# Kernel tuning notes

Measured on AMD Instinct MI355X. Metric: run time of the kernel, lower is better.

Reference implementation:

```python
import jax, jax.numpy as jnp
import numpy as np

N = 50000   # num_nodes
E = 400000  # num_edges
IN, HID, OUT, H = 128, 64, 128, 4
GAT_HID = HID * H  # 256
EPS = 1e-5
NEG_SLOPE = 0.2


def setup_inputs() -> dict:
    key = jax.random.key(0)
    ks = jax.random.split(key, 24)

    def w(k, shape, fan_in):
        return (jax.random.normal(k, shape) * (1.0 / np.sqrt(fan_in))).astype(jnp.float32)

    x = jax.random.normal(ks[0], (N, IN), dtype=jnp.float32)
    edge_index = jax.random.randint(ks[1], (2, E), 0, N, dtype=jnp.int32)

    return {
        "x": x,
        "edge_index": edge_index,
        # GCN branch: layer1 IN->HID, layer2 HID->OUT
        "W_gcn1": w(ks[2], (IN, HID), IN), "b_gcn1": jnp.zeros((HID,), jnp.float32),
        "W_gcn2": w(ks[3], (HID, OUT), HID), "b_gcn2": jnp.zeros((OUT,), jnp.float32),
        # GAT branch: layer1 IN -> H heads x HID (concat), layer2 GAT_HID -> H heads x OUT (mean)
        "W_gat1": w(ks[4], (IN, H * HID), IN),
        "a_src1": w(ks[5], (H, HID), HID), "a_dst1": w(ks[6], (H, HID), HID),
        "b_gat1": jnp.zeros((H * HID,), jnp.float32),
        "W_gat2": w(ks[7], (GAT_HID, H * OUT), GAT_HID),
        "a_src2": w(ks[8], (H, OUT), OUT), "a_dst2": w(ks[9], (H, OUT), OUT),
        "b_gat2": jnp.zeros((OUT,), jnp.float32),
        # LayerNorms
        "g_gcn": jnp.ones((OUT,), jnp.float32), "bt_gcn": jnp.zeros((OUT,), jnp.float32),
        "g_gat": jnp.ones((OUT,), jnp.float32), "bt_gat": jnp.zeros((OUT,), jnp.float32),
        # projected_concat fusion
        "W_fuse": w(ks[10], (2 * OUT, OUT), 2 * OUT), "b_fuse": jnp.zeros((OUT,), jnp.float32),
    }


def _with_self_loops(src, dst, n):
    loop = jnp.arange(n, dtype=src.dtype)
    return jnp.concatenate([src, loop]), jnp.concatenate([dst, loop])


def _gcn_layer(x, W, b, src, dst, n):
    # PyG GCNConv: x' = D^{-1/2}(A+I)D^{-1/2} X W + b
    xw = x @ W
    s, d = _with_self_loops(src, dst, n)
    deg = jax.ops.segment_sum(jnp.ones_like(s, dtype=xw.dtype), d, num_segments=n)
    dis = jnp.where(deg > 0, jax.lax.rsqrt(jnp.maximum(deg, 1.0)), 0.0)
    norm = dis[s] * dis[d]                      # [E2]
    msg = norm[:, None] * xw[s]                 # [E2, C]
    return jax.ops.segment_sum(msg, d, num_segments=n) + b


def _segment_softmax(e, seg, n):
    m = jax.ops.segment_max(e, seg, num_segments=n)
    ee = jnp.exp(e - m[seg])
    den = jax.ops.segment_sum(ee, seg, num_segments=n)
    return ee / den[seg]


def _gat_layer(x, W, a_src, a_dst, b, src, dst, n, heads, out_ch, concat):
    xh = (x @ W).reshape(n, heads, out_ch)      # [N, H, C]
    alpha_s = jnp.einsum('nhc,hc->nh', xh, a_src)
    alpha_d = jnp.einsum('nhc,hc->nh', xh, a_dst)
    s, d = _with_self_loops(src, dst, n)
    e = jax.nn.leaky_relu(alpha_s[s] + alpha_d[d], NEG_SLOPE)   # [E2, H]
    alpha = _segment_softmax(e, d, n)                           # [E2, H]
    out = jax.ops.segment_sum(alpha[:, :, None] * xh[s], d, num_segments=n)  # [N,H,C]
    if concat:
        return out.reshape(n, heads * out_ch) + b
    return out.mean(axis=1) + b


def _layer_norm(x, g, b):
    mu = x.mean(axis=-1, keepdims=True)
    var = ((x - mu) ** 2).mean(axis=-1, keepdims=True)
    return (x - mu) * jax.lax.rsqrt(var + EPS) * g + b


def reference(x, edge_index,
              W_gcn1, b_gcn1, W_gcn2, b_gcn2,
              W_gat1, a_src1, a_dst1, b_gat1,
              W_gat2, a_src2, a_dst2, b_gat2,
              g_gcn, bt_gcn, g_gat, bt_gat,
              W_fuse, b_fuse):
    src, dst = edge_index[0], edge_index[1]
    n = x.shape[0]
    # GCN branch (relu between layers, dropout p=0.0 -> identity)
    h = jax.nn.relu(_gcn_layer(x, W_gcn1, b_gcn1, src, dst, n))
    x_gcn = _gcn_layer(h, W_gcn2, b_gcn2, src, dst, n)
    # GAT branch (elu between layers)
    g1 = _gat_layer(x, W_gat1, a_src1, a_dst1, b_gat1, src, dst, n, H, HID, True)
    g1 = jax.nn.elu(g1)
    x_gat = _gat_layer(g1, W_gat2, a_src2, a_dst2, b_gat2, src, dst, n, H, OUT, False)
    # Norm + projected_concat fusion
    x_gcn = _layer_norm(x_gcn, g_gcn, bt_gcn)
    x_gat = _layer_norm(x_gat, g_gat, bt_gat)
    x_cat = jnp.concatenate([x_gcn, x_gat], axis=-1)
    return x_cat @ W_fuse + b_fuse
```

## Files before the change

kernel.cpp:

```cpp
#include <hip/hip_runtime.h>
#include <cmath>

static constexpr float EPS = 1e-5f;
static constexpr float NEG = 0.2f;

typedef __attribute__((ext_vector_type(8))) short short8v;
typedef __attribute__((ext_vector_type(4))) short short4v;
typedef __attribute__((ext_vector_type(4))) float f32x4;

__device__ inline unsigned short f2bf(float f) {
    union { float f; unsigned u; } v; v.f = f;
    unsigned r = v.u + 0x7FFF + ((v.u >> 16) & 1);
    return (unsigned short)(r >> 16);
}
__device__ inline float bf2f(unsigned short u) {
    union { unsigned u; float f; } v; v.u = (unsigned)u << 16; return v.f;
}

__global__ void count_kernel(const int* __restrict__ ei, int* __restrict__ cnt, int E) {
    int e = blockIdx.x * 256 + threadIdx.x;
    if (e < E) atomicAdd(&cnt[ei[E + e]], 1);
}

__global__ __launch_bounds__(256) void partial_kernel(const int* __restrict__ cnt,
                                                      int* __restrict__ partials, int n) {
    int tid = threadIdx.x, lane = tid & 63, wid = tid >> 6;
    int base = blockIdx.x * 1024 + tid * 4;
    int s = 0;
    if (base + 3 < n) {
        int4 v = *reinterpret_cast<const int4*>(&cnt[base]);
        s = v.x + v.y + v.z + v.w;
    } else {
        for (int j = 0; j < 4; j++) if (base + j < n) s += cnt[base + j];
    }
    #pragma unroll
    for (int o = 32; o; o >>= 1) s += __shfl_xor(s, o, 64);
    __shared__ int ws[4];
    if (lane == 0) ws[wid] = s;
    __syncthreads();
    if (tid == 0) partials[blockIdx.x] = ws[0] + ws[1] + ws[2] + ws[3];
}

__global__ void scanp_kernel(int* __restrict__ partials, int nb) {
    int lane = threadIdx.x;
    int v = (lane < nb) ? partials[lane] : 0;
    int s = v;
    #pragma unroll
    for (int o = 1; o < 64; o <<= 1) {
        int t = __shfl_up(s, o, 64);
        if (lane >= o) s += t;
    }
    if (lane < nb) partials[lane] = s - v;
}

__global__ __launch_bounds__(256) void scan2_kernel(const int* __restrict__ cnt,
                                                    const int* __restrict__ partials,
                                                    int* __restrict__ rowptr,
                                                    int* __restrict__ cursor,
                                                    float* __restrict__ dis, int n, int E) {
    int tid = threadIdx.x, lane = tid & 63, wid = tid >> 6;
    int base = blockIdx.x * 1024 + tid * 4;
    int v[4]; int s = 0;
    #pragma unroll
    for (int j = 0; j < 4; j++) { v[j] = (base + j < n) ? cnt[base + j] : 0; s += v[j]; }
    int ts = s;
    #pragma unroll
    for (int o = 1; o < 64; o <<= 1) {
        int t = __shfl_up(ts, o, 64);
        if (lane >= o) ts += t;
    }
    __shared__ int wsum[4];
    if (lane == 63) wsum[wid] = ts;
    __syncthreads();
    int woff = 0;
    for (int w = 0; w < wid; w++) woff += wsum[w];
    int excl = ts - s + woff + partials[blockIdx.x];
    #pragma unroll
    for (int j = 0; j < 4; j++) {
        int idx = base + j;
        if (idx < n) {
            rowptr[idx] = excl;
            cursor[idx] = excl;
            dis[idx] = rsqrtf((float)(v[j] + 1));
            excl += v[j];
        }
    }
    if (blockIdx.x == 0 && tid == 0) rowptr[n] = E;
}

__global__ void fill_kernel(const int* __restrict__ ei, int* __restrict__ cursor,
                            int* __restrict__ col, int E) {
    int e = blockIdx.x * 256 + threadIdx.x;
    if (e < E) {
        int d = ei[E + e];
        int pos = atomicAdd(&cursor[d], 1);
        col[pos] = ei[e];
    }
}

__global__ void convert_x_kernel(const float* __restrict__ x, unsigned short* __restrict__ xb, int total4) {
    int i = blockIdx.x * 256 + threadIdx.x;
    if (i < total4) {
        float4 v = *reinterpret_cast<const float4*>(&x[(size_t)i * 4]);
        unsigned long long pk = (unsigned long long)f2bf(v.x)
                              | ((unsigned long long)f2bf(v.y) << 16)
                              | ((unsigned long long)f2bf(v.z) << 32)
                              | ((unsigned long long)f2bf(v.w) << 48);
        *reinterpret_cast<unsigned long long*>(&xb[(size_t)i * 4]) = pk;
    }
}

__global__ void convert_weights_kernel(const float* W1, const float* W2, const float* W3,
                                       const float* W4, const float* W5,
                                       unsigned short* T1, unsigned short* T2, unsigned short* T3,
                                       unsigned short* T4, unsigned short* T5) {
    int idx = blockIdx.x * 256 + threadIdx.x;
    const float* S; unsigned short* D; int K, C, off;
    if      (idx <   8192) { S = W1; D = T1; K = 128; C =  64; off = 0; }
    else if (idx <  16384) { S = W2; D = T2; K =  64; C = 128; off = 8192; }
    else if (idx <  49152) { S = W3; D = T3; K = 128; C = 256; off = 16384; }
    else if (idx < 180224) { S = W4; D = T4; K = 256; C = 512; off = 49152; }
    else if (idx < 212992) { S = W5; D = T5; K = 256; C = 128; off = 180224; }
    else return;
    int j = idx - off;
    int c = j / K, k = j % K;
    D[j] = f2bf(S[(size_t)k * C + c]);
}

template<int K, int C, bool OBF>
__global__ __launch_bounds__(256) void mfma_gemm(const unsigned short* __restrict__ A,
                                                 const unsigned short* __restrict__ WT,
                                                 const float* __restrict__ bias,
                                                 void* __restrict__ outp, int M) {
    constexpr int BM = 128, BN = 64, BK = 64;
    __shared__ unsigned short As[BM * BK];
    __shared__ unsigned short Ws[BN * BK];
    int tid = threadIdx.x;
    int wid = tid >> 6, lane = tid & 63;
    int m0 = blockIdx.x * BM;
    int n0 = blockIdx.y * BN;

    f32x4 acc[2][4] = {};

    for (int k0 = 0; k0 < K; k0 += BK) {
        for (int i = tid; i < BM * (BK / 8); i += 256) {
            int row = i >> 3;
            int kk = (i & 7) * 8;
            int gr = m0 + row;
            short8v v = short8v{0, 0, 0, 0, 0, 0, 0, 0};
            if (gr < M) v = *reinterpret_cast<const short8v*>(&A[(size_t)gr * K + k0 + kk]);
            int byte = (kk * 2) ^ ((row & 7) << 4);
            *reinterpret_cast<short8v*>((char*)As + row * (BK * 2) + byte) = v;
        }
        for (int i = tid; i < BN * (BK / 8); i += 256) {
            int nrow = i >> 3;
            int kk = (i & 7) * 8;
            short8v v = *reinterpret_cast<const short8v*>(&WT[(size_t)(n0 + nrow) * K + k0 + kk]);
            int byte = (kk * 2) ^ ((nrow & 7) << 4);
            *reinterpret_cast<short8v*>((char*)Ws + nrow * (BK * 2) + byte) = v;
        }
        __syncthreads();
        #pragma unroll
        for (int kc = 0; kc < BK; kc += 32) {
            short8v afr[2], bfr[4];
            int kk = kc + (lane >> 4) * 8;
            #pragma unroll
            for (int mf = 0; mf < 2; mf++) {
                int row = wid * 32 + mf * 16 + (lane & 15);
                int byte = (kk * 2) ^ ((row & 7) << 4);
                afr[mf] = *reinterpret_cast<const short8v*>((char*)As + row * (BK * 2) + byte);
            }
            #pragma unroll
            for (int nf = 0; nf < 4; nf++) {
                int nrow = nf * 16 + (lane & 15);
                int byte = (kk * 2) ^ ((nrow & 7) << 4);
                bfr[nf] = *reinterpret_cast<const short8v*>((char*)Ws + nrow * (BK * 2) + byte);
            }
            #pragma unroll
            for (int mf = 0; mf < 2; mf++)
                #pragma unroll
                for (int nf = 0; nf < 4; nf++)
                    acc[mf][nf] = __builtin_amdgcn_mfma_f32_16x16x32_bf16(
                        afr[mf], bfr[nf], acc[mf][nf], 0, 0, 0);
        }
        __syncthreads();
    }
    #pragma unroll
    for (int mf = 0; mf < 2; mf++) {
        #pragma unroll
        for (int nf = 0; nf < 4; nf++) {
            #pragma unroll
            for (int r = 0; r < 4; r++) {
                int row = m0 + wid * 32 + mf * 16 + (lane >> 4) * 4 + r;
                int colg = n0 + nf * 16 + (lane & 15);
                if (row < M) {
                    float v = acc[mf][nf][r];
                    if (bias) v += bias[colg];
                    if constexpr (OBF)
                        ((unsigned short*)outp)[(size_t)row * C + colg] = f2bf(v);
                    else
                        ((float*)outp)[(size_t)row * C + colg] = v;
                }
            }
        }
    }
}

__global__ __launch_bounds__(256) void gcn_prop1_kernel(const unsigned short* __restrict__ xw,
                                                        const float* __restrict__ dis,
                                                        const int* __restrict__ rowptr,
                                                        const int* __restrict__ col,
                                                        const float* __restrict__ bias,
                                                        unsigned short* __restrict__ outp, int n) {
    int wid = threadIdx.x >> 6, lane = threadIdx.x & 63;
    int node = blockIdx.x * 4 + wid;
    if (node >= n) return;
    float dd = dis[node];
    float acc = dd * bf2f(xw[(size_t)node * 64 + lane]);
    int b0 = rowptr[node], b1 = rowptr[node + 1];
    for (int i = b0; i < b1; i++) {
        int s = col[i];
        acc += dis[s] * bf2f(xw[(size_t)s * 64 + lane]);
    }
    float r = dd * acc + bias[lane];
    r = fmaxf(r, 0.f);
    outp[(size_t)node * 64 + lane] = f2bf(r);
}

__global__ __launch_bounds__(256) void gcn_prop2_ln_kernel(const unsigned short* __restrict__ xw,
                                                           const float* __restrict__ dis,
                                                           const int* __restrict__ rowptr,
                                                           const int* __restrict__ col,
                                                           const float* __restrict__ bias,
                                                           const float* __restrict__ gw,
                                                           const float* __restrict__ gb,
                                                           unsigned short* __restrict__ catb, int n) {
    int wid = threadIdx.x >> 6, lane = threadIdx.x & 63;
    int node = blockIdx.x * 4 + wid;
    if (node >= n) return;
    float dd = dis[node];
    unsigned vs = *reinterpret_cast<const unsigned*>(&xw[(size_t)node * 128 + lane * 2]);
    float a0 = dd * bf2f((unsigned short)(vs & 0xFFFF));
    float a1 = dd * bf2f((unsigned short)(vs >> 16));
    int b0 = rowptr[node], b1 = rowptr[node + 1];
    for (int i = b0; i < b1; i++) {
        int s = col[i];
        float ds = dis[s];
        unsigned v = *reinterpret_cast<const unsigned*>(&xw[(size_t)s * 128 + lane * 2]);
        a0 += ds * bf2f((unsigned short)(v & 0xFFFF));
        a1 += ds * bf2f((unsigned short)(v >> 16));
    }
    float r0 = dd * a0 + bias[lane * 2];
    float r1 = dd * a1 + bias[lane * 2 + 1];
    float sm = r0 + r1, sq = r0 * r0 + r1 * r1;
    #pragma unroll
    for (int o = 1; o < 64; o <<= 1) { sm += __shfl_xor(sm, o, 64); sq += __shfl_xor(sq, o, 64); }
    float mu = sm * (1.f / 128.f);
    float var = sq * (1.f / 128.f) - mu * mu;
    float rs = rsqrtf(var + EPS);
    float o0 = (r0 - mu) * rs * gw[lane * 2] + gb[lane * 2];
    float o1 = (r1 - mu) * rs * gw[lane * 2 + 1] + gb[lane * 2 + 1];
    unsigned pk = (unsigned)f2bf(o0) | ((unsigned)f2bf(o1) << 16);
    *reinterpret_cast<unsigned*>(&catb[(size_t)node * 256 + lane * 2]) = pk;
}

template<int HC>
__global__ __launch_bounds__(256) void alpha_kernel(const unsigned short* __restrict__ xh,
                                                    const float* __restrict__ a_src,
                                                    const float* __restrict__ a_dst,
                                                    float* __restrict__ as_, float* __restrict__ ad_, int n) {
    constexpr int PL = HC / 16;
    int wid = threadIdx.x >> 6, lane = threadIdx.x & 63;
    int node = blockIdx.x * 4 + wid;
    if (node >= n) return;
    int head = lane >> 4, cb = (lane & 15) * PL;
    const unsigned short* xr = xh + (size_t)node * (4 * HC) + lane * PL;
    float ps = 0.f, pd = 0.f;
    #pragma unroll
    for (int j = 0; j < PL; j++) {
        float v = bf2f(xr[j]);
        ps += v * a_src[head * HC + cb + j];
        pd += v * a_dst[head * HC + cb + j];
    }
    #pragma unroll
    for (int o = 1; o < 16; o <<= 1) { ps += __shfl_xor(ps, o, 64); pd += __shfl_xor(pd, o, 64); }
    if ((lane & 15) == 0) {
        as_[(size_t)node * 4 + head] = ps;
        ad_[(size_t)node * 4 + head] = pd;
    }
}

__global__ __launch_bounds__(256) void gat_prop1_kernel(const unsigned short* __restrict__ xh,
                                                        const float* __restrict__ as_,
                                                        const float* __restrict__ ad_,
                                                        const int* __restrict__ rowptr,
                                                        const int* __restrict__ col,
                                                        const float* __restrict__ bias,
                                                        unsigned short* __restrict__ outp, int n) {
    constexpr int CAP = 96;
    __shared__ float ex[4][CAP][4];
    __shared__ int scol[4][CAP];
    int wid = threadIdx.x >> 6, lane = threadIdx.x & 63;
    int node = blockIdx.x * 4 + wid;
    if (node >= n) return;
    int b0 = rowptr[node];
    int cnt = rowptr[node + 1] - b0;
    float4 adv = *reinterpret_cast<const float4*>(&ad_[(size_t)node * 4]);
    float p0 = 0, p1 = 0, p2 = 0, p3 = 0;
    for (int i = lane; i <= cnt; i += 64) {
        int s = (i == cnt) ? node : col[b0 + i];
        float4 asv = *reinterpret_cast<const float4*>(&as_[(size_t)s * 4]);
        float e0 = asv.x + adv.x; e0 = e0 > 0.f ? e0 : NEG * e0; float x0 = __expf(e0);
        float e1 = asv.y + adv.y; e1 = e1 > 0.f ? e1 : NEG * e1; float x1 = __expf(e1);
        float e2 = asv.z + adv.z; e2 = e2 > 0.f ? e2 : NEG * e2; float x2 = __expf(e2);
        float e3 = asv.w + adv.w; e3 = e3 > 0.f ? e3 : NEG * e3; float x3 = __expf(e3);
        if (i < CAP) {
            ex[wid][i][0] = x0; ex[wid][i][1] = x1; ex[wid][i][2] = x2; ex[wid][i][3] = x3;
            scol[wid][i] = s;
        }
        p0 += x0; p1 += x1; p2 += x2; p3 += x3;
    }
    #pragma unroll
    for (int o = 1; o < 64; o <<= 1) {
        p0 += __shfl_xor(p0, o, 64); p1 += __shfl_xor(p1, o, 64);
        p2 += __shfl_xor(p2, o, 64); p3 += __shfl_xor(p3, o, 64);
    }
    __builtin_amdgcn_wave_barrier();
    int head = lane >> 4;
    float wsel = head == 0 ? 1.f / p0 : head == 1 ? 1.f / p1 : head == 2 ? 1.f / p2 : 1.f / p3;
    int coff = lane * 4;
    float fa0 = 0, fa1 = 0, fa2 = 0, fa3 = 0;
    for (int i = 0; i <= cnt; i++) {
        int s; float we;
        if (i < CAP) {
            s = scol[wid][i];
            we = ex[wid][i][head] * wsel;
        } else {
            s = (i == cnt) ? node : col[b0 + i];
            float4 asv = *reinterpret_cast<const float4*>(&as_[(size_t)s * 4]);
            float eh = head == 0 ? asv.x + adv.x : head == 1 ? asv.y + adv.y
                     : head == 2 ? asv.z + adv.z : asv.w + adv.w;
            eh = eh > 0.f ? eh : NEG * eh;
            we = __expf(eh) * wsel;
        }
        short4v v = *reinterpret_cast<const short4v*>(&xh[(size_t)s * 256 + coff]);
        fa0 += we * bf2f((unsigned short)v[0]);
        fa1 += we * bf2f((unsigned short)v[1]);
        fa2 += we * bf2f((unsigned short)v[2]);
        fa3 += we * bf2f((unsigned short)v[3]);
    }
    float r0 = fa0 + bias[coff];     r0 = r0 > 0.f ? r0 : __expf(r0) - 1.f;
    float r1 = fa1 + bias[coff + 1]; r1 = r1 > 0.f ? r1 : __expf(r1) - 1.f;
    float r2 = fa2 + bias[coff + 2]; r2 = r2 > 0.f ? r2 : __expf(r2) - 1.f;
    float r3 = fa3 + bias[coff + 3]; r3 = r3 > 0.f ? r3 : __expf(r3) - 1.f;
    short4v o4;
    o4[0] = (short)f2bf(r0); o4[1] = (short)f2bf(r1);
    o4[2] = (short)f2bf(r2); o4[3] = (short)f2bf(r3);
    *reinterpret_cast<short4v*>(&outp[(size_t)node * 256 + coff]) = o4;
}

__global__ __launch_bounds__(256) void gat_prop2_ln_kernel(const unsigned short* __restrict__ xh,
                                                           const float* __restrict__ as_,
                                                           const float* __restrict__ ad_,
                                                           const int* __restrict__ rowptr,
                                                           const int* __restrict__ col,
                                                           const float* __restrict__ bias,
                                                           const float* __restrict__ gw,
                                                           const float* __restrict__ gb,
                                                           unsigned short* __restrict__ catb, int n) {
    constexpr int CAP = 96;
    __shared__ float ex[4][CAP][4];
    __shared__ int scol[4][CAP];
    int wid = threadIdx.x >> 6, lane = threadIdx.x & 63;
    int node = blockIdx.x * 4 + wid;
    if (node >= n) return;
    int b0 = rowptr[node];
    int cnt = rowptr[node + 1] - b0;
    float4 adv = *reinterpret_cast<const float4*>(&ad_[(size_t)node * 4]);
    float p0 = 0, p1 = 0, p2 = 0, p3 = 0;
    for (int i = lane; i <= cnt; i += 64) {
        int s = (i == cnt) ? node : col[b0 + i];
        float4 asv = *reinterpret_cast<const float4*>(&as_[(size_t)s * 4]);
        float e0 = asv.x + adv.x; e0 = e0 > 0.f ? e0 : NEG * e0; float x0 = __expf(e0);
        float e1 = asv.y + adv.y; e1 = e1 > 0.f ? e1 : NEG * e1; float x1 = __expf(e1);
        float e2 = asv.z + adv.z; e2 = e2 > 0.f ? e2 : NEG * e2; float x2 = __expf(e2);
        float e3 = asv.w + adv.w; e3 = e3 > 0.f ? e3 : NEG * e3; float x3 = __expf(e3);
        if (i < CAP) {
            ex[wid][i][0] = x0; ex[wid][i][1] = x1; ex[wid][i][2] = x2; ex[wid][i][3] = x3;
            scol[wid][i] = s;
        }
        p0 += x0; p1 += x1; p2 += x2; p3 += x3;
    }
    #pragma unroll
    for (int o = 1; o < 64; o <<= 1) {
        p0 += __shfl_xor(p0, o, 64); p1 += __shfl_xor(p1, o, 64);
        p2 += __shfl_xor(p2, o, 64); p3 += __shfl_xor(p3, o, 64);
    }
    __builtin_amdgcn_wave_barrier();
    int head = lane >> 4;
    float wsel = head == 0 ? 0.25f / p0 : head == 1 ? 0.25f / p1 : head == 2 ? 0.25f / p2 : 0.25f / p3;
    int cw = (lane & 15) * 8;
    float facc[8] = {0, 0, 0, 0, 0, 0, 0, 0};
    for (int i = 0; i <= cnt; i++) {
        int s; float we;
        if (i < CAP) {
            s = scol[wid][i];
            we = ex[wid][i][head] * wsel;
        } else {
            s = (i == cnt) ? node : col[b0 + i];
            float4 asv = *reinterpret_cast<const float4*>(&as_[(size_t)s * 4]);
            float eh = head == 0 ? asv.x + adv.x : head == 1 ? asv.y + adv.y
                     : head == 2 ? asv.z + adv.z : asv.w + adv.w;
            eh = eh > 0.f ? eh : NEG * eh;
            we = __expf(eh) * wsel;
        }
        short8v v = *reinterpret_cast<const short8v*>(&xh[(size_t)s * 512 + lane * 8]);
        #pragma unroll
        for (int j = 0; j < 8; j++) facc[j] += we * bf2f((unsigned short)v[j]);
    }
    #pragma unroll
    for (int j = 0; j < 8; j++) {
        facc[j] += __shfl_xor(facc[j], 16, 64);
        facc[j] += __shfl_xor(facc[j], 32, 64);
        facc[j] += bias[cw + j];
    }
    float sm = 0, sq = 0;
    #pragma unroll
    for (int j = 0; j < 8; j++) { sm += facc[j]; sq += facc[j] * facc[j]; }
    #pragma unroll
    for (int o = 1; o < 16; o <<= 1) { sm += __shfl_xor(sm, o, 64); sq += __shfl_xor(sq, o, 64); }
    float mu = sm * (1.f / 128.f);
    float var = sq * (1.f / 128.f) - mu * mu;
    float rs = rsqrtf(var + EPS);
    if (lane < 16) {
        short8v o8;
        #pragma unroll
        for (int j = 0; j < 8; j++)
            o8[j] = (short)f2bf((facc[j] - mu) * rs * gw[cw + j] + gb[cw + j]);
        *reinterpret_cast<short8v*>(&catb[(size_t)node * 256 + 128 + cw]) = o8;
    }
}

extern "C" void kernel_launch(void* const* d_in, const int* in_sizes, int n_in,
                              void* d_out, int out_size, void* d_ws, size_t ws_size,
                              hipStream_t stream) {
    const float* x      = (const float*)d_in[0];
    const int*   ei     = (const int*)d_in[1];
    const float* W_gcn1 = (const float*)d_in[2];
    const float* b_gcn1 = (const float*)d_in[3];
    const float* W_gcn2 = (const float*)d_in[4];
    const float* b_gcn2 = (const float*)d_in[5];
    const float* W_gat1 = (const float*)d_in[6];
    const float* a_src1 = (const float*)d_in[7];
    const float* a_dst1 = (const float*)d_in[8];
    const float* b_gat1 = (const float*)d_in[9];
    const float* W_gat2 = (const float*)d_in[10];
    const float* a_src2 = (const float*)d_in[11];
    const float* a_dst2 = (const float*)d_in[12];
    const float* b_gat2 = (const float*)d_in[13];
    const float* g_gcn  = (const float*)d_in[14];
    const float* bt_gcn = (const float*)d_in[15];
    const float* g_gat  = (const float*)d_in[16];
    const float* bt_gat = (const float*)d_in[17];
    const float* W_fuse = (const float*)d_in[18];
    const float* b_fuse = (const float*)d_in[19];
    float* out = (float*)d_out;

    const int n = in_sizes[0] / 128;
    const int E = in_sizes[1] / 2;

    char* ws = (char*)d_ws;
    size_t off = 0;
    auto alloc = [&](size_t bytes) -> char* {
        char* p = ws + off;
        off += (bytes + 255) & ~(size_t)255;
        return p;
    };
    int*   cnt      = (int*)alloc((size_t)n * 4);
    int*   rowptr   = (int*)alloc((size_t)(n + 1) * 4);
    int*   cursor   = (int*)alloc((size_t)n * 4);
    int*   col      = (int*)alloc((size_t)E * 4);
    int*   partials = (int*)alloc(64 * 4);
    float* dis      = (float*)alloc((size_t)n * 4);
    float* as_      = (float*)alloc((size_t)n * 16);
    float* ad_      = (float*)alloc((size_t)n * 16);
    unsigned short* xb   = (unsigned short*)alloc((size_t)n * 128 * 2);
    unsigned short* WT1  = (unsigned short*)alloc(8192 * 2);
    unsigned short* WT2  = (unsigned short*)alloc(8192 * 2);
    unsigned short* WT3  = (unsigned short*)alloc(32768 * 2);
    unsigned short* WT4  = (unsigned short*)alloc(131072 * 2);
    unsigned short* WT5  = (unsigned short*)alloc(32768 * 2);
    unsigned short* xw1b = (unsigned short*)alloc((size_t)n * 64 * 2);
    unsigned short* hb   = (unsigned short*)alloc((size_t)n * 64 * 2);
    unsigned short* xw2b = (unsigned short*)alloc((size_t)n * 128 * 2);
    unsigned short* xh1b = (unsigned short*)alloc((size_t)n * 256 * 2);
    unsigned short* g1b  = (unsigned short*)alloc((size_t)n * 256 * 2);
    unsigned short* xh2b = (unsigned short*)alloc((size_t)n * 512 * 2);
    unsigned short* catb = (unsigned short*)alloc((size_t)n * 256 * 2);

    const int nb = (n + 1023) / 1024;

    hipMemsetAsync(cnt, 0, (size_t)n * 4, stream);
    count_kernel<<<(E + 255) / 256, 256, 0, stream>>>(ei, cnt, E);
    partial_kernel<<<nb, 256, 0, stream>>>(cnt, partials, n);
    scanp_kernel<<<1, 64, 0, stream>>>(partials, nb);
    scan2_kernel<<<nb, 256, 0, stream>>>(cnt, partials, rowptr, cursor, dis, n, E);
    fill_kernel<<<(E + 255) / 256, 256, 0, stream>>>(ei, cursor, col, E);
    convert_x_kernel<<<(n * 32 + 255) / 256, 256, 0, stream>>>(x, xb, n * 32);
    convert_weights_kernel<<<(212992 + 255) / 256, 256, 0, stream>>>(
        W_gcn1, W_gcn2, W_gat1, W_gat2, W_fuse, WT1, WT2, WT3, WT4, WT5);

    int gm = (n + 127) / 128;
    int gn4 = (n + 3) / 4;

    mfma_gemm<128, 64, true><<<dim3(gm, 1), 256, 0, stream>>>(xb, WT1, nullptr, xw1b, n);
    gcn_prop1_kernel<<<gn4, 256, 0, stream>>>(xw1b, dis, rowptr, col, b_gcn1, hb, n);
    mfma_gemm<64, 128, true><<<dim3(gm, 2), 256, 0, stream>>>(hb, WT2, nullptr, xw2b, n);
    gcn_prop2_ln_kernel<<<gn4, 256, 0, stream>>>(xw2b, dis, rowptr, col, b_gcn2, g_gcn, bt_gcn, catb, n);

    mfma_gemm<128, 256, true><<<dim3(gm, 4), 256, 0, stream>>>(xb, WT3, nullptr, xh1b, n);
    alpha_kernel<64><<<gn4, 256, 0, stream>>>(xh1b, a_src1, a_dst1, as_, ad_, n);
    gat_prop1_kernel<<<gn4, 256, 0, stream>>>(xh1b, as_, ad_, rowptr, col, b_gat1, g1b, n);
    mfma_gemm<256, 512, true><<<dim3(gm, 8), 256, 0, stream>>>(g1b, WT4, nullptr, xh2b, n);
    alpha_kernel<128><<<gn4, 256, 0, stream>>>(xh2b, a_src2, a_dst2, as_, ad_, n);
    gat_prop2_ln_kernel<<<gn4, 256, 0, stream>>>(xh2b, as_, ad_, rowptr, col, b_gat2, g_gat, bt_gat, catb, n);

    mfma_gemm<256, 128, false><<<dim3(gm, 2), 256, 0, stream>>>(catb, WT5, b_fuse, out, n);
}
```

Baseline: 394.3 us.

## Reorder GAT layers to aggregate first, then transform with fused epilogues

Both GAT layers now aggregate neighbour features before the linear projection, instead of projecting and then aggregating. The gather per edge therefore runs over the narrower input width (128 and 256) rather than the projected width (256 and 512). Attention logits are computed straight from the inputs using precomputed products of W and the attention vectors. ELU, bias, head mean and LayerNorm are folded into the following GEMM epilogues. In exchange, per-head aggregated buffers as wide as 1024 bf16 per node must be written and read, and the second GEMM's K grows to 1024.

Result: slower. 444.8 us (+12.8%).

```diff
diff --git a/kernel.cpp b/kernel.cpp
--- a/kernel.cpp
+++ b/kernel.cpp
@@ -113,18 +113,47 @@
 __global__ void convert_weights_kernel(const float* W1, const float* W2, const float* W3,
                                        const float* W4, const float* W5,
                                        unsigned short* T1, unsigned short* T2, unsigned short* T3,
-                                       unsigned short* T4, unsigned short* T5) {
+                                       unsigned short* TF, unsigned short* T5) {
     int idx = blockIdx.x * 256 + threadIdx.x;
-    const float* S; unsigned short* D; int K, C, off;
-    if      (idx <   8192) { S = W1; D = T1; K = 128; C =  64; off = 0; }
-    else if (idx <  16384) { S = W2; D = T2; K =  64; C = 128; off = 8192; }
-    else if (idx <  49152) { S = W3; D = T3; K = 128; C = 256; off = 16384; }
-    else if (idx < 180224) { S = W4; D = T4; K = 256; C = 512; off = 49152; }
-    else if (idx < 212992) { S = W5; D = T5; K = 256; C = 128; off = 180224; }
-    else return;
-    int j = idx - off;
-    int c = j / K, k = j % K;
-    D[j] = f2bf(S[(size_t)k * C + c]);
+    if (idx < 8192) {
+        int j = idx, c = j / 128, k = j % 128;
+        T1[j] = f2bf(W1[(size_t)k * 64 + c]);
+    } else if (idx < 16384) {
+        int j = idx - 8192, c = j / 64, k = j % 64;
+        T2[j] = f2bf(W2[(size_t)k * 128 + c]);
+    } else if (idx < 49152) {
+        int j = idx - 16384, c = j / 128, k = j % 128;
+        T3[j] = f2bf(W3[(size_t)k * 256 + c]);
+    } else if (idx < 180224) {
+        int j = idx - 49152;
+        int c = j / 1024, kk = j % 1024, h = kk >> 8, k = kk & 255;
+        TF[j] = f2bf(0.25f * W4[(size_t)k * 512 + h * 128 + c]);
+    } else if (idx < 212992) {
+        int j = idx - 180224, c = j / 256, k = j % 256;
+        T5[j] = f2bf(W5[(size_t)k * 128 + c]);
+    }
+}
+
+__global__ void walpha_kernel(const float* __restrict__ W1, const float* __restrict__ as1,
+                              const float* __restrict__ ad1,
+                              const float* __restrict__ W2, const float* __restrict__ as2,
+                              const float* __restrict__ ad2,
+                              float* __restrict__ wa1, float* __restrict__ wa2) {
+    int idx = blockIdx.x * 256 + threadIdx.x;
+    if (idx < 1024) {
+        int k = idx >> 3, t = idx & 7, h = t >> 1;
+        const float* a = (t & 1) ? ad1 : as1;
+        float s = 0.f;
+        for (int c = 0; c < 64; c++) s += W1[(size_t)k * 256 + h * 64 + c] * a[h * 64 + c];
+        wa1[idx] = s;
+    } else if (idx < 3072) {
+        int j = idx - 1024;
+        int k = j >> 3, t = j & 7, h = t >> 1;
+        const float* a = (t & 1) ? ad2 : as2;
+        float s = 0.f;
+        for (int c = 0; c < 128; c++) s += W2[(size_t)k * 512 + h * 128 + c] * a[h * 128 + c];
+        wa2[j] = s;
+    }
 }
 
 template<int K, int C, bool OBF>
@@ -201,6 +230,174 @@
                     else
                         ((float*)outp)[(size_t)row * C + colg] = v;
                 }
+            }
+        }
+    }
+}
+
+__global__ __launch_bounds__(256) void gemm_head_kernel(const unsigned short* __restrict__ A,
+                                                        const unsigned short* __restrict__ WT3,
+                                                        const float* __restrict__ bias,
+                                                        unsigned short* __restrict__ g1b, int M) {
+    constexpr int BM = 128, BK = 64, K = 128;
+    int head = blockIdx.y;
+    __shared__ unsigned short As[BM * BK];
+    __shared__ unsigned short Ws[64 * BK];
+    int tid = threadIdx.x;
+    int wid = tid >> 6, lane = tid & 63;
+    int m0 = blockIdx.x * BM;
+
+    f32x4 acc[2][4] = {};
+
+    for (int k0 = 0; k0 < K; k0 += BK) {
+        for (int i = tid; i < BM * (BK / 8); i += 256) {
+            int row = i >> 3;
+            int kk = (i & 7) * 8;
+            int gr = m0 + row;
+            short8v v = short8v{0, 0, 0, 0, 0, 0, 0, 0};
+            if (gr < M) v = *reinterpret_cast<const short8v*>(&A[(size_t)gr * 512 + head * 128 + k0 + kk]);
+            int byte = (kk * 2) ^ ((row & 7) << 4);
+            *reinterpret_cast<short8v*>((char*)As + row * (BK * 2) + byte) = v;
+        }
+        for (int i = tid; i < 64 * (BK / 8); i += 256) {
+            int nrow = i >> 3;
+            int kk = (i & 7) * 8;
+            short8v v = *reinterpret_cast<const short8v*>(&WT3[(size_t)(head * 64 + nrow) * 128 + k0 + kk]);
+            int byte = (kk * 2) ^ ((nrow & 7) << 4);
+            *reinterpret_cast<short8v*>((char*)Ws + nrow * (BK * 2) + byte) = v;
+        }
+        __syncthreads();
+        #pragma unroll
+        for (int kc = 0; kc < BK; kc += 32) {
+            short8v afr[2], bfr[4];
+            int kk = kc + (lane >> 4) * 8;
+            #pragma unroll
+            for (int mf = 0; mf < 2; mf++) {
+                int row = wid * 32 + mf * 16 + (lane & 15);
+                int byte = (kk * 2) ^ ((row & 7) << 4);
+                afr[mf] = *reinterpret_cast<const short8v*>((char*)As + row * (BK * 2) + byte);
+            }
+            #pragma unroll
+            for (int nf = 0; nf < 4; nf++) {
+                int nrow = nf * 16 + (lane & 15);
+                int byte = (kk * 2) ^ ((nrow & 7) << 4);
+                bfr[nf] = *reinterpret_cast<const short8v*>((char*)Ws + nrow * (BK * 2) + byte);
+            }
+            #pragma unroll
+            for (int mf = 0; mf < 2; mf++)
+                #pragma unroll
+                for (int nf = 0; nf < 4; nf++)
+                    acc[mf][nf] = __builtin_amdgcn_mfma_f32_16x16x32_bf16(
+                        afr[mf], bfr[nf], acc[mf][nf], 0, 0, 0);
+        }
+        __syncthreads();
+    }
+    #pragma unroll
+    for (int mf = 0; mf < 2; mf++) {
+        #pragma unroll
+        for (int nf = 0; nf < 4; nf++) {
+            #pragma unroll
+            for (int r = 0; r < 4; r++) {
+                int row = m0 + wid * 32 + mf * 16 + (lane >> 4) * 4 + r;
+                int cl = head * 64 + nf * 16 + (lane & 15);
+                if (row < M) {
+                    float v = acc[mf][nf][r] + bias[cl];
+                    v = v > 0.f ? v : __expf(v) - 1.f;
+                    g1b[(size_t)row * 256 + cl] = f2bf(v);
+                }
+            }
+        }
+    }
+}
+
+template<int K>
+__global__ __launch_bounds__(256) void gemm_ln_kernel(const unsigned short* __restrict__ A,
+                                                      const unsigned short* __restrict__ WT,
+                                                      const float* __restrict__ bias,
+                                                      const float* __restrict__ gw,
+                                                      const float* __restrict__ gb,
+                                                      unsigned short* __restrict__ catb,
+                                                      int coloff, int M) {
+    constexpr int BM = 128, BN = 128, BK = 64;
+    __shared__ unsigned short As[BM * BK];
+    __shared__ unsigned short Ws[BN * BK];
+    int tid = threadIdx.x;
+    int wid = tid >> 6, lane = tid & 63;
+    int m0 = blockIdx.x * BM;
+
+    f32x4 acc[2][8] = {};
+
+    for (int k0 = 0; k0 < K; k0 += BK) {
+        for (int i = tid; i < BM * (BK / 8); i += 256) {
+            int row = i >> 3;
+            int kk = (i & 7) * 8;
+            int gr = m0 + row;
+            short8v v = short8v{0, 0, 0, 0, 0, 0, 0, 0};
+            if (gr < M) v = *reinterpret_cast<const short8v*>(&A[(size_t)gr * K + k0 + kk]);
+            int byte = (kk * 2) ^ ((row & 7) << 4);
+            *reinterpret_cast<short8v*>((char*)As + row * (BK * 2) + byte) = v;
+        }
+        for (int i = tid; i < BN * (BK / 8); i += 256) {
+            int nrow = i >> 3;
+            int kk = (i & 7) * 8;
+            short8v v = *reinterpret_cast<const short8v*>(&WT[(size_t)nrow * K + k0 + kk]);
+            int byte = (kk * 2) ^ ((nrow & 7) << 4);
+            *reinterpret_cast<short8v*>((char*)Ws + nrow * (BK * 2) + byte) = v;
+        }
+        __syncthreads();
+        #pragma unroll
+        for (int kc = 0; kc < BK; kc += 32) {
+            short8v afr[2], bfr[8];
+            int kk = kc + (lane >> 4) * 8;
+            #pragma unroll
+            for (int mf = 0; mf < 2; mf++) {
+                int row = wid * 32 + mf * 16 + (lane & 15);
+                int byte = (kk * 2) ^ ((row & 7) << 4);
+                afr[mf] = *reinterpret_cast<const short8v*>((char*)As + row * (BK * 2) + byte);
+            }
+            #pragma unroll
+            for (int nf = 0; nf < 8; nf++) {
+                int nrow = nf * 16 + (lane & 15);
+                int byte = (kk * 2) ^ ((nrow & 7) << 4);
+                bfr[nf] = *reinterpret_cast<const short8v*>((char*)Ws + nrow * (BK * 2) + byte);
+            }
+            #pragma unroll
+            for (int mf = 0; mf < 2; mf++)
+                #pragma unroll
+                for (int nf = 0; nf < 8; nf++)
+                    acc[mf][nf] = __builtin_amdgcn_mfma_f32_16x16x32_bf16(
+                        afr[mf], bfr[nf], acc[mf][nf], 0, 0, 0);
+        }
+        __syncthreads();
+    }
+    int cb = lane & 15;
+    float gwv[8], gbv[8], bv[8];
+    #pragma unroll
+    for (int nf = 0; nf < 8; nf++) {
+        int c = nf * 16 + cb;
+        gwv[nf] = gw[c]; gbv[nf] = gb[c]; bv[nf] = bias[c];
+    }
+    #pragma unroll
+    for (int mf = 0; mf < 2; mf++) {
+        #pragma unroll
+        for (int r = 0; r < 4; r++) {
+            int row = m0 + wid * 32 + mf * 16 + (lane >> 4) * 4 + r;
+            float v[8]; float sm = 0.f, sq = 0.f;
+            #pragma unroll
+            for (int nf = 0; nf < 8; nf++) {
+                v[nf] = acc[mf][nf][r] + bv[nf];
+                sm += v[nf]; sq += v[nf] * v[nf];
+            }
+            #pragma unroll
+            for (int o = 1; o < 16; o <<= 1) { sm += __shfl_xor(sm, o, 64); sq += __shfl_xor(sq, o, 64); }
+            float mu = sm * (1.f / 128.f);
+            float var = sq * (1.f / 128.f) - mu * mu;
+            float rs = rsqrtf(var + EPS);
+            if (row < M) {
+                #pragma unroll
+                for (int nf = 0; nf < 8; nf++)
+                    catb[(size_t)row * 256 + coloff + nf * 16 + cb] =
+                        f2bf((v[nf] - mu) * rs * gwv[nf] + gbv[nf]);
             }
         }
     }
@@ -264,39 +461,44 @@
     *reinterpret_cast<unsigned*>(&catb[(size_t)node * 256 + lane * 2]) = pk;
 }
 
-template<int HC>
-__global__ __launch_bounds__(256) void alpha_kernel(const unsigned short* __restrict__ xh,
-                                                    const float* __restrict__ a_src,
-                                                    const float* __restrict__ a_dst,
-                                                    float* __restrict__ as_, float* __restrict__ ad_, int n) {
-    constexpr int PL = HC / 16;
+template<int K>
+__global__ __launch_bounds__(256) void alpha_x_kernel(const unsigned short* __restrict__ F,
+                                                      const float* __restrict__ wa,
+                                                      float* __restrict__ as_, float* __restrict__ ad_, int n) {
+    constexpr int PL = K / 64;
     int wid = threadIdx.x >> 6, lane = threadIdx.x & 63;
     int node = blockIdx.x * 4 + wid;
     if (node >= n) return;
-    int head = lane >> 4, cb = (lane & 15) * PL;
-    const unsigned short* xr = xh + (size_t)node * (4 * HC) + lane * PL;
-    float ps = 0.f, pd = 0.f;
+    float p[8] = {0, 0, 0, 0, 0, 0, 0, 0};
+    const unsigned short* fr = F + (size_t)node * K + lane * PL;
     #pragma unroll
     for (int j = 0; j < PL; j++) {
-        float v = bf2f(xr[j]);
-        ps += v * a_src[head * HC + cb + j];
-        pd += v * a_dst[head * HC + cb + j];
-    }
-    #pragma unroll
-    for (int o = 1; o < 16; o <<= 1) { ps += __shfl_xor(ps, o, 64); pd += __shfl_xor(pd, o, 64); }
-    if ((lane & 15) == 0) {
-        as_[(size_t)node * 4 + head] = ps;
-        ad_[(size_t)node * 4 + head] = pd;
-    }
-}
-
-__global__ __launch_bounds__(256) void gat_prop1_kernel(const unsigned short* __restrict__ xh,
-                                                        const float* __restrict__ as_,
-                                                        const float* __restrict__ ad_,
-                                                        const int* __restrict__ rowptr,
-                                                        const int* __restrict__ col,
-                                                        const float* __restrict__ bias,
-                                                        unsigned short* __restrict__ outp, int n) {
+        float v = bf2f(fr[j]);
+        const float4* w4 = reinterpret_cast<const float4*>(wa + (size_t)(lane * PL + j) * 8);
+        float4 wA = w4[0], wB = w4[1];
+        p[0] += v * wA.x; p[1] += v * wA.y; p[2] += v * wA.z; p[3] += v * wA.w;
+        p[4] += v * wB.x; p[5] += v * wB.y; p[6] += v * wB.z; p[7] += v * wB.w;
+    }
+    #pragma unroll
+    for (int o = 1; o < 64; o <<= 1) {
+        #pragma unroll
+        for (int t = 0; t < 8; t++) p[t] += __shfl_xor(p[t], o, 64);
+    }
+    if (lane == 0) {
+        #pragma unroll
+        for (int t = 0; t < 8; t++) {
+            if (t & 1) ad_[(size_t)node * 4 + (t >> 1)] = p[t];
+            else       as_[(size_t)node * 4 + (t >> 1)] = p[t];
+        }
+    }
+}
+
+__global__ __launch_bounds__(256) void gat_agg1_kernel(const unsigned short* __restrict__ xb,
+                                                       const float* __restrict__ as_,
+                                                       const float* __restrict__ ad_,
+                                                       const int* __restrict__ rowptr,
+                                                       const int* __restrict__ col,
+                                                       unsigned short* __restrict__ agg, int n) {
     constexpr int CAP = 96;
     __shared__ float ex[4][CAP][4];
     __shared__ int scol[4][CAP];
@@ -326,48 +528,45 @@
         p2 += __shfl_xor(p2, o, 64); p3 += __shfl_xor(p3, o, 64);
     }
     __builtin_amdgcn_wave_barrier();
-    int head = lane >> 4;
-    float wsel = head == 0 ? 1.f / p0 : head == 1 ? 1.f / p1 : head == 2 ? 1.f / p2 : 1.f / p3;
-    int coff = lane * 4;
-    float fa0 = 0, fa1 = 0, fa2 = 0, fa3 = 0;
+    float inv0 = 1.f / p0, inv1 = 1.f / p1, inv2 = 1.f / p2, inv3 = 1.f / p3;
+    float ac[4][2] = {};
     for (int i = 0; i <= cnt; i++) {
-        int s; float we;
+        int s; float w0, w1, w2, w3;
         if (i < CAP) {
             s = scol[wid][i];
-            we = ex[wid][i][head] * wsel;
+            float4 e = *reinterpret_cast<const float4*>(&ex[wid][i][0]);
+            w0 = e.x * inv0; w1 = e.y * inv1; w2 = e.z * inv2; w3 = e.w * inv3;
         } else {
             s = (i == cnt) ? node : col[b0 + i];
             float4 asv = *reinterpret_cast<const float4*>(&as_[(size_t)s * 4]);
-            float eh = head == 0 ? asv.x + adv.x : head == 1 ? asv.y + adv.y
-                     : head == 2 ? asv.z + adv.z : asv.w + adv.w;
-            eh = eh > 0.f ? eh : NEG * eh;
-            we = __expf(eh) * wsel;
-        }
-        short4v v = *reinterpret_cast<const short4v*>(&xh[(size_t)s * 256 + coff]);
-        fa0 += we * bf2f((unsigned short)v[0]);
-        fa1 += we * bf2f((unsigned short)v[1]);
-        fa2 += we * bf2f((unsigned short)v[2]);
-        fa3 += we * bf2f((unsigned short)v[3]);
-    }
-    float r0 = fa0 + bias[coff];     r0 = r0 > 0.f ? r0 : __expf(r0) - 1.f;
-    float r1 = fa1 + bias[coff + 1]; r1 = r1 > 0.f ? r1 : __expf(r1) - 1.f;
-    float r2 = fa2 + bias[coff + 2]; r2 = r2 > 0.f ? r2 : __expf(r2) - 1.f;
-    float r3 = fa3 + bias[coff + 3]; r3 = r3 > 0.f ? r3 : __expf(r3) - 1.f;
-    short4v o4;
-    o4[0] = (short)f2bf(r0); o4[1] = (short)f2bf(r1);
-    o4[2] = (short)f2bf(r2); o4[3] = (short)f2bf(r3);
-    *reinterpret_cast<short4v*>(&outp[(size_t)node * 256 + coff]) = o4;
-}
-
-__global__ __launch_bounds__(256) void gat_prop2_ln_kernel(const unsigned short* __restrict__ xh,
-                                                           const float* __restrict__ as_,
-                                                           const float* __restrict__ ad_,
-                                                           const int* __restrict__ rowptr,
-                                                           const int* __restrict__ col,
-                                                           const float* __restrict__ bias,
-                                                           const float* __restrict__ gw,
-                                                           const float* __restrict__ gb,
-                                                           unsigned short* __restrict__ catb, int n) {
+            float e0 = asv.x + adv.x; e0 = e0 > 0.f ? e0 : NEG * e0;
+            float e1 = asv.y + adv.y; e1 = e1 > 0.f ? e1 : NEG * e1;
+            float e2 = asv.z + adv.z; e2 = e2 > 0.f ? e2 : NEG * e2;
+            float e3 = asv.w + adv.w; e3 = e3 > 0.f ? e3 : NEG * e3;
+            w0 = __expf(e0) * inv0; w1 = __expf(e1) * inv1;
+            w2 = __expf(e2) * inv2; w3 = __expf(e3) * inv3;
+        }
+        unsigned v = *reinterpret_cast<const unsigned*>(&xb[(size_t)s * 128 + lane * 2]);
+        float f0 = bf2f((unsigned short)(v & 0xFFFF));
+        float f1 = bf2f((unsigned short)(v >> 16));
+        ac[0][0] += w0 * f0; ac[0][1] += w0 * f1;
+        ac[1][0] += w1 * f0; ac[1][1] += w1 * f1;
+        ac[2][0] += w2 * f0; ac[2][1] += w2 * f1;
+        ac[3][0] += w3 * f0; ac[3][1] += w3 * f1;
+    }
+    #pragma unroll
+    for (int h = 0; h < 4; h++) {
+        unsigned pk = (unsigned)f2bf(ac[h][0]) | ((unsigned)f2bf(ac[h][1]) << 16);
+        *reinterpret_cast<unsigned*>(&agg[(size_t)node * 512 + h * 128 + lane * 2]) = pk;
+    }
+}
+
+__global__ __launch_bounds__(256) void gat_agg2_kernel(const unsigned short* __restrict__ g1b,
+                                                       const float* __restrict__ as_,
+                                                       const float* __restrict__ ad_,
+                                                       const int* __restrict__ rowptr,
+                                                       const int* __restrict__ col,
+                                                       unsigned short* __restrict__ agg, int n) {
     constexpr int CAP = 96;
     __shared__ float ex[4][CAP][4];
     __shared__ int scol[4][CAP];
@@ -397,47 +596,40 @@
         p2 += __shfl_xor(p2, o, 64); p3 += __shfl_xor(p3, o, 64);
     }
     __builtin_amdgcn_wave_barrier();
-    int head = lane >> 4;
-    float wsel = head == 0 ? 0.25f / p0 : head == 1 ? 0.25f / p1 : head == 2 ? 0.25f / p2 : 0.25f / p3;
-    int cw = (lane & 15) * 8;
-    float facc[8] = {0, 0, 0, 0, 0, 0, 0, 0};
+    float inv0 = 1.f / p0, inv1 = 1.f / p1, inv2 = 1.f / p2, inv3 = 1.f / p3;
+    float ac[4][4] = {};
     for (int i = 0; i <= cnt; i++) {
-        int s; float we;
+        int s; float w0, w1, w2, w3;
         if (i < CAP) {
             s = scol[wid][i];
-            we = ex[wid][i][head] * wsel;
+            float4 e = *reinterpret_cast<const float4*>(&ex[wid][i][0]);
+            w0 = e.x * inv0; w1 = e.y * inv1; w2 = e.z * inv2; w3 = e.w * inv3;
         } else {
             s = (i == cnt) ? node : col[b0 + i];
             float4 asv = *reinterpret_cast<const float4*>(&as_[(size_t)s * 4]);
-            float eh = head == 0 ? asv.x + adv.x : head == 1 ? asv.y + adv.y
-                     : head == 2 ? asv.z + adv.z : asv.w + adv.w;
-            eh = eh > 0.f ? eh : NEG * eh;
-            we = __expf(eh) * wsel;
-        }
-        short8v v = *reinterpret_cast<const short8v*>(&xh[(size_t)s * 512 + lane * 8]);
-        #pragma unroll
-        for (int j = 0; j < 8; j++) facc[j] += we * bf2f((unsigned short)v[j]);
-    }
-    #pragma unroll
-    for (int j = 0; j < 8; j++) {
-        facc[j] += __shfl_xor(facc[j], 16, 64);
-        facc[j] += __shfl_xor(facc[j], 32, 64);
-        facc[j] += bias[cw + j];
-    }
-    float sm = 0, sq = 0;
-    #pragma unroll
-    for (int j = 0; j < 8; j++) { sm += facc[j]; sq += facc[j] * facc[j]; }
-    #pragma unroll
-    for (int o = 1; o < 16; o <<= 1) { sm += __shfl_xor(sm, o, 64); sq += __shfl_xor(sq, o, 64); }
-    float mu = sm * (1.f / 128.f);
-    float var = sq * (1.f / 128.f) - mu * mu;
-    float rs = rsqrtf(var + EPS);
-    if (lane < 16) {
-        short8v o8;
-        #pragma unroll
-        for (int j = 0; j < 8; j++)
-            o8[j] = (short)f2bf((facc[j] - mu) * rs * gw[cw + j] + gb[cw + j]);
-        *reinterpret_cast<short8v*>(&catb[(size_t)node * 256 + 128 + cw]) = o8;
+            float e0 = asv.x + adv.x; e0 = e0 > 0.f ? e0 : NEG * e0;
+            float e1 = asv.y + adv.y; e1 = e1 > 0.f ? e1 : NEG * e1;
+            float e2 = asv.z + adv.z; e2 = e2 > 0.f ? e2 : NEG * e2;
+            float e3 = asv.w + adv.w; e3 = e3 > 0.f ? e3 : NEG * e3;
+            w0 = __expf(e0) * inv0; w1 = __expf(e1) * inv1;
+            w2 = __expf(e2) * inv2; w3 = __expf(e3) * inv3;
+        }
+        short4v v = *reinterpret_cast<const short4v*>(&g1b[(size_t)s * 256 + lane * 4]);
+        float f0 = bf2f((unsigned short)v[0]);
+        float f1 = bf2f((unsigned short)v[1]);
+        float f2 = bf2f((unsigned short)v[2]);
+        float f3 = bf2f((unsigned short)v[3]);
+        ac[0][0] += w0 * f0; ac[0][1] += w0 * f1; ac[0][2] += w0 * f2; ac[0][3] += w0 * f3;
+        ac[1][0] += w1 * f0; ac[1][1] += w1 * f1; ac[1][2] += w1 * f2; ac[1][3] += w1 * f3;
+        ac[2][0] += w2 * f0; ac[2][1] += w2 * f1; ac[2][2] += w2 * f2; ac[2][3] += w2 * f3;
+        ac[3][0] += w3 * f0; ac[3][1] += w3 * f1; ac[3][2] += w3 * f2; ac[3][3] += w3 * f3;
+    }
+    #pragma unroll
+    for (int h = 0; h < 4; h++) {
+        short4v o4;
+        o4[0] = (short)f2bf(ac[h][0]); o4[1] = (short)f2bf(ac[h][1]);
+        o4[2] = (short)f2bf(ac[h][2]); o4[3] = (short)f2bf(ac[h][3]);
+        *reinterpret_cast<short4v*>(&agg[(size_t)node * 1024 + h * 256 + lane * 4]) = o4;
     }
 }
 
@@ -484,18 +676,21 @@
     float* dis      = (float*)alloc((size_t)n * 4);
     float* as_      = (float*)alloc((size_t)n * 16);
     float* ad_      = (float*)alloc((size_t)n * 16);
+    float* wa1      = (float*)alloc(1024 * 4);
+    float* wa2      = (float*)alloc(2048 * 4);
     unsigned short* xb   = (unsigned short*)alloc((size_t)n * 128 * 2);
     unsigned short* WT1  = (unsigned short*)alloc(8192 * 2);
     unsigned short* WT2  = (unsigned short*)alloc(8192 * 2);
     unsigned short* WT3  = (unsigned short*)alloc(32768 * 2);
-    unsigned short* WT4  = (unsigned short*)alloc(131072 * 2);
+    unsigned short* WTF  = (unsigned short*)alloc(131072 * 2);
     unsigned short* WT5  = (unsigned short*)alloc(32768 * 2);
-    unsigned short* xw1b = (unsigned short*)alloc((size_t)n * 64 * 2);
-    unsigned short* hb   = (unsigned short*)alloc((size_t)n * 64 * 2);
-    unsigned short* xw2b = (unsigned short*)alloc((size_t)n * 128 * 2);
-    unsigned short* xh1b = (unsigned short*)alloc((size_t)n * 256 * 2);
+    unsigned short* BIG  = (unsigned short*)alloc((size_t)n * 1024 * 2);
+    unsigned short* agg1b = BIG;
+    unsigned short* agg2b = BIG;
+    unsigned short* xw1b = BIG + (size_t)n * 512;
+    unsigned short* hb   = xw1b + (size_t)n * 64;
+    unsigned short* xw2b = hb + (size_t)n * 64;
     unsigned short* g1b  = (unsigned short*)alloc((size_t)n * 256 * 2);
-    unsigned short* xh2b = (unsigned short*)alloc((size_t)n * 512 * 2);
     unsigned short* catb = (unsigned short*)alloc((size_t)n * 256 * 2);
 
     const int nb = (n + 1023) / 1024;
@@ -508,7 +703,8 @@
     fill_kernel<<<(E + 255) / 256, 256, 0, stream>>>(ei, cursor, col, E);
     convert_x_kernel<<<(n * 32 + 255) / 256, 256, 0, stream>>>(x, xb, n * 32);
     convert_weights_kernel<<<(212992 + 255) / 256, 256, 0, stream>>>(
-        W_gcn1, W_gcn2, W_gat1, W_gat2, W_fuse, WT1, WT2, WT3, WT4, WT5);
+        W_gcn1, W_gcn2, W_gat1, W_gat2, W_fuse, WT1, WT2, WT3, WTF, WT5);
+    walpha_kernel<<<12, 256, 0, stream>>>(W_gat1, a_src1, a_dst1, W_gat2, a_src2, a_dst2, wa1, wa2);
 
     int gm = (n + 127) / 128;
     int gn4 = (n + 3) / 4;
@@ -518,12 +714,12 @@
     mfma_gemm<64, 128, true><<<dim3(gm, 2), 256, 0, stream>>>(hb, WT2, nullptr, xw2b, n);
     gcn_prop2_ln_kernel<<<gn4, 256, 0, stream>>>(xw2b, dis, rowptr, col, b_gcn2, g_gcn, bt_gcn, catb, n);
 
-    mfma_gemm<128, 256, true><<<dim3(gm, 4), 256, 0, stream>>>(xb, WT3, nullptr, xh1b, n);
-    alpha_kernel<64><<<gn4, 256, 0, stream>>>(xh1b, a_src1, a_dst1, as_, ad_, n);
-    gat_prop1_kernel<<<gn4, 256, 0, stream>>>(xh1b, as_, ad_, rowptr, col, b_gat1, g1b, n);
-    mfma_gemm<256, 512, true><<<dim3(gm, 8), 256, 0, stream>>>(g1b, WT4, nullptr, xh2b, n);
-    alpha_kernel<128><<<gn4, 256, 0, stream>>>(xh2b, a_src2, a_dst2, as_, ad_, n);
-    gat_prop2_ln_kernel<<<gn4, 256, 0, stream>>>(xh2b, as_, ad_, rowptr, col, b_gat2, g_gat, bt_gat, catb, n);
+    alpha_x_kernel<128><<<gn4, 256, 0, stream>>>(xb, wa1, as_, ad_, n);
+    gat_agg1_kernel<<<gn4, 256, 0, stream>>>(xb, as_, ad_, rowptr, col, agg1b, n);
+    gemm_head_kernel<<<dim3(gm, 4), 256, 0, stream>>>(agg1b, WT3, b_gat1, g1b, n);
+    alpha_x_kernel<256><<<gn4, 256, 0, stream>>>(g1b, wa2, as_, ad_, n);
+    gat_agg2_kernel<<<gn4, 256, 0, stream>>>(g1b, as_, ad_, rowptr, col, agg2b, n);
+    gemm_ln_kernel<1024><<<gm, 256, 0, stream>>>(agg2b, WTF, b_gat2, g_gat, bt_gat, catb, 128, n);
 
     mfma_gemm<256, 128, false><<<dim3(gm, 2), 256, 0, stream>>>(catb, WT5, b_fuse, out, n);
 }
```
